# Kernel tuning notes

Measured on AMD Instinct MI355X. Metric: run time of the kernel, lower is better.

## Reference

```python
import jax, jax.numpy as jnp
import numpy as np

N, E = 50000, 800000
IN_DIM, DIM, MP_STEPS, POS_DIM = 64, 128, 3, 3
EPS = 1e-5


def _ln(v):
    # LayerNorm without affine params (elementwise_affine=False)
    m = jnp.mean(v, axis=-1, keepdims=True)
    var = jnp.mean((v - m) ** 2, axis=-1, keepdims=True)
    return (v - m) * jax.lax.rsqrt(var + EPS)


def setup_inputs() -> dict:
    key = jax.random.key(0)
    ks = jax.random.split(key, 10)
    x = jax.random.normal(ks[0], (N, IN_DIM), dtype=jnp.float32)
    pos = jax.random.normal(ks[1], (N, POS_DIM), dtype=jnp.float32)
    edge_index = jax.random.randint(ks[2], (2, E), 0, N, dtype=jnp.int64)
    # Linear embed: torch Linear stores [out,in]; we store transposed [in,out]
    s_e = 1.0 / np.sqrt(IN_DIM)
    embed_w = jax.random.uniform(ks[3], (IN_DIM, DIM), jnp.float32, -s_e, s_e)
    embed_b = jax.random.uniform(ks[4], (DIM,), jnp.float32, -s_e, s_e)
    s_m = 1.0 / np.sqrt(2 * DIM + POS_DIM)
    msg_w = jax.random.uniform(ks[5], (MP_STEPS, 2 * DIM + POS_DIM, DIM), jnp.float32, -s_m, s_m)
    msg_b = jax.random.uniform(ks[6], (MP_STEPS, DIM), jnp.float32, -s_m, s_m)
    s_u = 1.0 / np.sqrt(2 * DIM)
    upd_w = jax.random.uniform(ks[7], (MP_STEPS, 2 * DIM, DIM), jnp.float32, -s_u, s_u)
    upd_b = jax.random.uniform(ks[8], (MP_STEPS, DIM), jnp.float32, -s_u, s_u)
    return {"x": x, "pos": pos, "edge_index": edge_index,
            "embed_w": embed_w, "embed_b": embed_b,
            "msg_w": msg_w, "msg_b": msg_b,
            "upd_w": upd_w, "upd_b": upd_b}


def reference(x, pos, edge_index, embed_w, embed_b, msg_w, msg_b, upd_w, upd_b):
    row, col = edge_index[0], edge_index[1]
    h = x @ embed_w + embed_b  # [N, DIM]
    # edge_attr computed under torch.no_grad -> constant
    edge_attr = jax.lax.stop_gradient(pos[row] - pos[col])  # [E, POS_DIM]
    ones = jnp.ones((E,), dtype=h.dtype)
    counts = jax.ops.segment_sum(ones, col, num_segments=N)  # [N]
    denom = jnp.maximum(counts, 1.0)[:, None]
    for s in range(MP_STEPS):
        mi = jnp.concatenate([h[row], h[col], edge_attr], axis=-1)  # [E, 2D+3]
        messages = _ln(jax.nn.gelu(mi @ msg_w[s] + msg_b[s], approximate=False))
        agg = jax.ops.segment_sum(messages, col, num_segments=N) / denom  # scatter_mean
        ui = jnp.concatenate([h, agg], axis=-1)  # [N, 2D]
        h = h + _ln(ui @ upd_w[s] + upd_b[s])
    return h
```

## Files before the change

### kernel.cpp

```cpp
#include <hip/hip_runtime.h>
#include <hip/hip_bf16.h>

#define NN 50000
#define NE 800000
#define IND 64
#define DIM 128
#define KUPD 256
#define NB_SCAN 196
#define NTILE 3125

typedef __attribute__((ext_vector_type(8))) short bf16x8;
typedef __attribute__((ext_vector_type(4))) short bf16x4;
typedef __attribute__((ext_vector_type(4))) float f32x4;
typedef __attribute__((ext_vector_type(2))) float f32x2;

static __device__ __forceinline__ short f2bf(float f) {
  union { __hip_bfloat16 b; short s; } u;
  u.b = __float2bfloat16(f);
  return u.s;
}
static __device__ __forceinline__ float bf2f(unsigned short u) {
  union { float f; unsigned int i; } x; x.i = ((unsigned int)u) << 16; return x.f;
}
static __device__ __forceinline__ float fexp2(float x) {
  float r; asm("v_exp_f32 %0, %1" : "=v"(r) : "v"(x)); return r;
}
static __device__ __forceinline__ float frcp(float x) {
  float r; asm("v_rcp_f32 %0, %1" : "=v"(r) : "v"(x)); return r;
}
static __device__ __forceinline__ float qsum16(float x) {
  x += __int_as_float(__builtin_amdgcn_mov_dpp(__float_as_int(x), 0x128, 0xf, 0xf, false));
  x += __int_as_float(__builtin_amdgcn_mov_dpp(__float_as_int(x), 0x124, 0xf, 0xf, false));
  x += __int_as_float(__builtin_amdgcn_mov_dpp(__float_as_int(x), 0x122, 0xf, 0xf, false));
  x += __int_as_float(__builtin_amdgcn_mov_dpp(__float_as_int(x), 0x121, 0xf, 0xf, false));
  return x;
}

__global__ __launch_bounds__(256) void embed_kernel(
    const float* __restrict__ x, const float* __restrict__ w,
    const float* __restrict__ b, short* __restrict__ hb) {
  __shared__ float ws[IND * DIM];
  __shared__ float xs[8 * IND];
  const int t = threadIdx.x;
  for (int i = t * 4; i < IND * DIM; i += 1024)
    *(float4*)(ws + i) = *(const float4*)(w + i);
  {
    int i = t * 4;
    if (i < 8 * IND)
      *(float4*)(xs + i) = *(const float4*)(x + (size_t)blockIdx.x * (8 * IND) + i);
  }
  __syncthreads();
  const int d = t & 127, g = t >> 7;
  const float bd = b[d];
  for (int nnod = g; nnod < 8; nnod += 2) {
    float acc = bd;
#pragma unroll
    for (int k = 0; k < IND; ++k) acc += xs[nnod * IND + k] * ws[k * DIM + d];
    const size_t n = (size_t)blockIdx.x * 8 + nnod;
    hb[n * DIM + d] = f2bf(acc);
  }
}

__global__ __launch_bounds__(256) void counts_kernel(const int* __restrict__ ei,
                                                     int* __restrict__ cnt) {
  int e = blockIdx.x * 256 + threadIdx.x;
  if (e < NE) atomicAdd(&cnt[ei[NE + e]], 1);
}

__global__ __launch_bounds__(256) void bsum_dhist_kernel(const int* __restrict__ cnt,
                                                         int* __restrict__ bsum,
                                                         int* __restrict__ dhist) {
  __shared__ int lh[64];
  __shared__ int wsum[4];
  int t = threadIdx.x, idx = blockIdx.x * 256 + t;
  if (t < 64) lh[t] = 0;
  __syncthreads();
  int c = (idx < NN) ? cnt[idx] : 0;
  int s = c;
#pragma unroll
  for (int m = 1; m < 64; m <<= 1) s += __shfl_xor(s, m, 64);
  if ((t & 63) == 0) wsum[t >> 6] = s;
  if (idx < NN) {
    int d = c > 63 ? 63 : c;
    atomicAdd(&lh[63 - d], 1);
  }
  __syncthreads();
  if (t == 0) bsum[blockIdx.x] = wsum[0] + wsum[1] + wsum[2] + wsum[3];
  if (t < 64 && lh[t] > 0) atomicAdd(&dhist[t], lh[t]);
}

__global__ __launch_bounds__(256) void bscan_dscan_kernel(const int* __restrict__ bsum,
                                                          int* __restrict__ boff,
                                                          const int* __restrict__ dhist,
                                                          int* __restrict__ dcur) {
  __shared__ int sh[256];
  int t = threadIdx.x;
  int v = (t < NB_SCAN) ? bsum[t] : 0;
  sh[t] = v;
  __syncthreads();
  for (int d = 1; d < 256; d <<= 1) {
    int u = (t >= d) ? sh[t - d] : 0;
    __syncthreads();
    sh[t] += u;
    __syncthreads();
  }
  if (t < NB_SCAN) boff[t] = sh[t] - v;
  if (t < 64) {
    int dv = dhist[t];
    int ds = dv;
    for (int d = 1; d < 64; d <<= 1) {
      int u = __shfl_up(ds, d, 64);
      if (t >= d) ds += u;
    }
    dcur[t] = ds - dv;
  }
}

__global__ __launch_bounds__(256) void final_scan_kernel(
    const int* __restrict__ cnt, const int* __restrict__ boff,
    int* __restrict__ dcur, const float* __restrict__ pos,
    int* __restrict__ off, int* __restrict__ cursor, float* __restrict__ rden,
    int* __restrict__ nodeOrd, float4* __restrict__ pos4g) {
  __shared__ int sh[256];
  __shared__ int lh[64];
  __shared__ int lbase[64];
  int b = blockIdx.x, t = threadIdx.x;
  int idx = b * 256 + t;
  bool act = (idx < NN);
  int c = act ? cnt[idx] : 0;
  if (t < 64) lh[t] = 0;
  sh[t] = c;
  __syncthreads();
  for (int d = 1; d < 256; d <<= 1) {
    int u = (t >= d) ? sh[t - d] : 0;
    __syncthreads();
    sh[t] += u;
    __syncthreads();
  }
  int bin = 63 - (c > 63 ? 63 : c);
  int lrank = 0;
  if (act) {
    int e = boff[b] + sh[t] - c;
    off[idx] = e;
    cursor[idx] = e;
    rden[idx] = 1.0f / fmaxf((float)c, 1.0f);
    pos4g[idx] = make_float4(pos[3 * idx], pos[3 * idx + 1], pos[3 * idx + 2], 0.f);
    lrank = atomicAdd(&lh[bin], 1);
  }
  __syncthreads();
  if (t < 64) lbase[t] = (lh[t] > 0) ? atomicAdd(&dcur[t], lh[t]) : 0;
  __syncthreads();
  if (act) nodeOrd[lbase[bin] + lrank] = idx;
  if (b == 0 && t == 0) off[NN] = NE;
}

__global__ __launch_bounds__(256) void scatter_kernel(const int* __restrict__ ei,
                                                      int* __restrict__ cursor,
                                                      int* __restrict__ rowOf) {
  int e = blockIdx.x * 256 + threadIdx.x;
  if (e < NE) {
    int c = ei[NE + e];
    int p = atomicAdd(&cursor[c], 1);
    rowOf[p] = ei[e];
  }
}

__global__ __launch_bounds__(256) void wt_all_kernel(const float* __restrict__ wm,
                                                     const float* __restrict__ wu,
                                                     short* __restrict__ wt12,
                                                     short* __restrict__ wtu) {
  int i = blockIdx.x * 256 + threadIdx.x;
  if (i < 3 * 256 * DIM) {
    int k = i % DIM, o = (i / DIM) % 256, s = i / (DIM * 256);
    int krow = (o < DIM) ? k : (DIM + k);
    int d = o & (DIM - 1);
    wt12[i] = f2bf(wm[((size_t)s * 259 + krow) * DIM + d]);
  } else {
    int j = i - 3 * 256 * DIM;
    if (j < 3 * DIM * KUPD) {
      int k = j % KUPD, d = (j / KUPD) % DIM, s = j / (KUPD * DIM);
      wtu[j] = f2bf(wu[((size_t)s * KUPD + k) * DIM + d]);
    }
  }
}

__global__ __launch_bounds__(512) void p12_kernel(const short* __restrict__ hb,
                                                  const short* __restrict__ wt12_s,
                                                  short* __restrict__ P12b) {
  __shared__ short wlds[256 * 132];
  const int t = threadIdx.x;
  const int wid = t >> 6, lane = t & 63;
  const int m = lane & 15, kg = lane >> 4;
  for (int i = t * 8; i < 256 * DIM; i += 512 * 8) {
    int r = i >> 7, c = i & 127;
    *(bf16x8*)(&wlds[r * 132 + c]) = *(const bf16x8*)(wt12_s + i);
  }
  __syncthreads();
  const int wgid = blockIdx.x * 8 + wid;
#pragma unroll
  for (int rep = 0; rep < 2; ++rep) {
    int tid = wgid + rep * 2048;
    if (tid >= NTILE) break;
    int nbase = tid * 16;
    const short* hrow = hb + (size_t)(nbase + m) * DIM;
    bf16x8 bfrag[4];
#pragma unroll
    for (int cc = 0; cc < 4; ++cc)
      bfrag[cc] = *(const bf16x8*)(hrow + cc * 32 + kg * 8);
#pragma unroll
    for (int half = 0; half < 2; ++half) {
      f32x4 acc[8];
#pragma unroll
      for (int i = 0; i < 8; ++i) acc[i] = (f32x4)0.0f;
#pragma unroll
      for (int cc = 0; cc < 4; ++cc) {
#pragma unroll
        for (int tl = 0; tl < 8; ++tl) {
          bf16x8 afrag = *(const bf16x8*)(&wlds[(half * DIM + tl * 16 + m) * 132 + cc * 32 + kg * 8]);
          acc[tl] = __builtin_amdgcn_mfma_f32_16x16x32_bf16(afrag, bfrag[cc], acc[tl], 0, 0, 0);
        }
      }
#pragma unroll
      for (int tl = 0; tl < 8; ++tl) {
        bf16x4 p;
#pragma unroll
        for (int j = 0; j < 4; ++j) p[j] = f2bf(acc[tl][j]);
        *(bf16x4*)(P12b + (size_t)(nbase + m) * 256 + half * DIM + tl * 16 + kg * 4) = p;
      }
    }
  }
}

__global__ __launch_bounds__(256) void msg_agg_kernel(
    const short* __restrict__ P12b, const float4* __restrict__ pos4g,
    const int* __restrict__ rowOf, const int* __restrict__ off,
    const int* __restrict__ nodeOrd, const float* __restrict__ rden,
    const float* __restrict__ wmsg_s,
    const float* __restrict__ bias_s, short* __restrict__ aggb) {
  const int t = threadIdx.x;
  const int wid = t >> 6, lane = t & 63;
  const int n = nodeOrd[blockIdx.x * 4 + wid];
  const int q = lane >> 4;
  const int d0 = (lane & 15) * 8;
  f32x2 w30v[4], w31v[4], w32v[4], pbv[4];
  {
    const float* w30p = wmsg_s + 256 * DIM + d0;
    const float* w31p = wmsg_s + 257 * DIM + d0;
    const float* w32p = wmsg_s + 258 * DIM + d0;
    bf16x8 p2v = *(const bf16x8*)(P12b + (size_t)n * 256 + DIM + d0);
#pragma unroll
    for (int p = 0; p < 4; ++p) {
      w30v[p] = *(const f32x2*)(w30p + 2 * p);
      w31v[p] = *(const f32x2*)(w31p + 2 * p);
      w32v[p] = *(const f32x2*)(w32p + 2 * p);
      f32x2 bb = *(const f32x2*)(bias_s + d0 + 2 * p);
      pbv[p].x = bf2f((unsigned short)p2v[2 * p]) + bb.x;
      pbv[p].y = bf2f((unsigned short)p2v[2 * p + 1]) + bb.y;
    }
  }
  const float4 pc = pos4g[n];
  const int start = off[n], end = off[n + 1];
  f32x2 av[4];
#pragma unroll
  for (int p = 0; p < 4; ++p) av[p] = (f32x2)0.0f;
  float bacc = 0.f;
  const f32x2 gc1 = (f32x2)(-0.102951604f);
  const f32x2 gc0 = (f32x2)(-2.30234934f);
  const f32x2 onev = (f32x2)1.0f;
  if (start < end) {
    const int last = end - 1;
    int ia = start + q; if (ia > last) ia = last;
    int ra = rowOf[ia];
    bf16x8 p1a = *(const bf16x8*)(P12b + (size_t)ra * 256 + d0);
    float4 ppa = pos4g[ra];
    int ib = start + 4 + q; if (ib > last) ib = last;
    int rb = rowOf[ib];
    bf16x8 p1b = *(const bf16x8*)(P12b + (size_t)rb * 256 + d0);
    float4 ppb = pos4g[rb];
#pragma unroll 2
    for (int jg = start; jg < end; jg += 4) {
      int ic = jg + 8 + q; if (ic > last) ic = last;
      int rc = rowOf[ic];
      bf16x8 p1c = *(const bf16x8*)(P12b + (size_t)rc * 256 + d0);
      float4 ppc = pos4g[rc];
      f32x2 e0v = (f32x2)(ppa.x - pc.x);
      f32x2 e1v = (f32x2)(ppa.y - pc.y);
      f32x2 e2v = (f32x2)(ppa.z - pc.z);
      f32x2 g[4];
      f32x2 s1v = (f32x2)0.0f, s2v = (f32x2)0.0f;
#pragma unroll
      for (int p = 0; p < 4; ++p) {
        unsigned int u = ((const unsigned int*)&p1a)[p];
        f32x2 v;
        v.x = __uint_as_float(u << 16);
        v.y = __uint_as_float(u & 0xffff0000u);
        v = v + pbv[p];
        v = __builtin_elementwise_fma(e2v, w32v[p], v);
        v = __builtin_elementwise_fma(e1v, w31v[p], v);
        v = __builtin_elementwise_fma(e0v, w30v[p], v);
        f32x2 u2 = v * v;
        f32x2 wv = __builtin_elementwise_fma(u2, gc1, gc0);
        f32x2 zv = v * wv;
        f32x2 tv;
        tv.x = fexp2(zv.x);
        tv.y = fexp2(zv.y);
        tv = tv + onev;
        f32x2 rv;
        rv.x = frcp(tv.x);
        rv.y = frcp(tv.y);
        f32x2 gg = v * rv;
        g[p] = gg;
        s1v = s1v + gg;
        s2v = __builtin_elementwise_fma(gg, gg, s2v);
      }
      float s1 = s1v.x + s1v.y;
      float s2 = s2v.x + s2v.y;
      s1 = qsum16(s1);
      s2 = qsum16(s2);
      float mean = s1 * (1.0f / 128.0f);
      float tvv = fmaf(mean, -mean, 1e-5f);
      float var = fmaf(s2, 1.0f / 128.0f, tvv);
      float rstd = rsqrtf(var);
      float rs = (jg + q < end) ? rstd : 0.0f;
      bacc = fmaf(mean, rs, bacc);
      f32x2 rsv = (f32x2)rs;
#pragma unroll
      for (int p = 0; p < 4; ++p) av[p] = __builtin_elementwise_fma(g[p], rsv, av[p]);
      p1a = p1b; ppa = ppb;
      p1b = p1c; ppb = ppc;
    }
  }
  const float rd = rden[n];
  float out[8];
#pragma unroll
  for (int p = 0; p < 4; ++p) {
    out[2 * p] = av[p].x - bacc;
    out[2 * p + 1] = av[p].y - bacc;
  }
  bf16x8 ob;
#pragma unroll
  for (int k = 0; k < 8; ++k) {
    out[k] += __shfl_xor(out[k], 16, 64);
    out[k] += __shfl_xor(out[k], 32, 64);
    ob[k] = f2bf(out[k] * rd);
  }
  if (q == 0)
    *(bf16x8*)(aggb + (size_t)n * DIM + d0) = ob;
}

template <int FINAL>
__global__ __launch_bounds__(512) void updp12_kernel(
    const short* hb, const short* __restrict__ aggb,
    const short* __restrict__ wtu_s,
    const short* __restrict__ wt12_n,
    const float* __restrict__ bias, float* __restrict__ h, short* hbo,
    short* __restrict__ P12b) {
  __shared__ short wlds[33792];
  const int t = threadIdx.x;
  const int wid = t >> 6, lane = t & 63;
  const int m = lane & 15, kg = lane >> 4;
  for (int i = t * 8; i < DIM * 256; i += 512 * 8) {
    int r = i >> 8, c = i & 255;
    *(bf16x8*)(&wlds[r * 264 + c]) = *(const bf16x8*)(wtu_s + i);
  }
  __syncthreads();
  const int wgid = blockIdx.x * 8 + wid;
#pragma unroll
  for (int rep = 0; rep < 2; ++rep) {
    int tid = wgid + rep * 2048;
    if (tid >= NTILE) break;
    int nbase = tid * 16;
    const int nA = nbase + m;
    const short* hrow = hb + (size_t)nA * DIM;
    const short* arow = aggb + (size_t)nA * DIM;

    f32x4 acc[8];
#pragma unroll
    for (int i = 0; i < 8; ++i) acc[i] = (f32x4)0.0f;
#pragma unroll
    for (int cc = 0; cc < 8; ++cc) {
      bf16x8 a = (cc < 4) ? *(const bf16x8*)(hrow + cc * 32 + kg * 8)
                          : *(const bf16x8*)(arow + (cc - 4) * 32 + kg * 8);
#pragma unroll
      for (int tl = 0; tl < 8; ++tl) {
        bf16x8 bfr = *(const bf16x8*)(&wlds[(tl * 16 + m) * 264 + cc * 32 + kg * 8]);
        acc[tl] = __builtin_amdgcn_mfma_f32_16x16x32_bf16(a, bfr, acc[tl], 0, 0, 0);
      }
    }

    float s1[4] = {0.f, 0.f, 0.f, 0.f}, s2[4] = {0.f, 0.f, 0.f, 0.f};
#pragma unroll
    for (int tl = 0; tl < 8; ++tl) {
      float bd = bias[tl * 16 + m];
#pragma unroll
      for (int j = 0; j < 4; ++j) {
        float xv = acc[tl][j] + bd;
        acc[tl][j] = xv;
        s1[j] += xv;
        s2[j] = fmaf(xv, xv, s2[j]);
      }
    }
#pragma unroll
    for (int mask = 1; mask < 16; mask <<= 1) {
#pragma unroll
      for (int j = 0; j < 4; ++j) {
        s1[j] += __shfl_xor(s1[j], mask, 64);
        s2[j] += __shfl_xor(s2[j], mask, 64);
      }
    }
#pragma unroll
    for (int j = 0; j < 4; ++j) {
      float mean = s1[j] * (1.0f / 128.0f);
      float var = s2[j] * (1.0f / 128.0f) - mean * mean;
      float rstd = rsqrtf(var + 1e-5f);
      int nw = nbase + kg * 4 + j;
#pragma unroll
      for (int tl = 0; tl < 8; ++tl) {
        int d = tl * 16 + m;
        float res = bf2f((unsigned short)hb[(size_t)nw * DIM + d]);
        float hv = res + (acc[tl][j] - mean) * rstd;
        if (FINAL) h[(size_t)nw * DIM + d] = hv;
        else       hbo[(size_t)nw * DIM + d] = f2bf(hv);
      }
    }
  }
  if (FINAL) return;

  __syncthreads();
  for (int i = t * 8; i < 256 * DIM; i += 512 * 8) {
    int r = i >> 7, c = i & 127;
    *(bf16x8*)(&wlds[r * 132 + c]) = *(const bf16x8*)(wt12_n + i);
  }
  __syncthreads();
#pragma unroll
  for (int rep = 0; rep < 2; ++rep) {
    int tid = wgid + rep * 2048;
    if (tid >= NTILE) break;
    int nbase = tid * 16;
    const short* hrow = hbo + (size_t)(nbase + m) * DIM;
    bf16x8 bfrag[4];
#pragma unroll
    for (int cc = 0; cc < 4; ++cc)
      bfrag[cc] = *(const bf16x8*)(hrow + cc * 32 + kg * 8);
#pragma unroll
    for (int half = 0; half < 2; ++half) {
      f32x4 acc[8];
#pragma unroll
      for (int i = 0; i < 8; ++i) acc[i] = (f32x4)0.0f;
#pragma unroll
      for (int cc = 0; cc < 4; ++cc) {
#pragma unroll
        for (int tl = 0; tl < 8; ++tl) {
          bf16x8 afrag = *(const bf16x8*)(&wlds[(half * DIM + tl * 16 + m) * 132 + cc * 32 + kg * 8]);
          acc[tl] = __builtin_amdgcn_mfma_f32_16x16x32_bf16(afrag, bfrag[cc], acc[tl], 0, 0, 0);
        }
      }
#pragma unroll
      for (int tl = 0; tl < 8; ++tl) {
        bf16x4 p;
#pragma unroll
        for (int j = 0; j < 4; ++j) p[j] = f2bf(acc[tl][j]);
        *(bf16x4*)(P12b + (size_t)(nbase + m) * 256 + half * DIM + tl * 16 + kg * 4) = p;
      }
    }
  }
}

extern "C" void kernel_launch(void* const* d_in, const int* in_sizes, int n_in,
                              void* d_out, int out_size, void* d_ws, size_t ws_size,
                              hipStream_t stream) {
  const float* x       = (const float*)d_in[0];
  const float* pos     = (const float*)d_in[1];
  const int* ei        = (const int*)d_in[2];
  const float* embed_w = (const float*)d_in[3];
  const float* embed_b = (const float*)d_in[4];
  const float* msg_w   = (const float*)d_in[5];
  const float* msg_b   = (const float*)d_in[6];
  const float* upd_w   = (const float*)d_in[7];
  const float* upd_b   = (const float*)d_in[8];
  float* h = (float*)d_out;

  char* ws = (char*)d_ws;
  size_t off_b = 0;
  short* hb     = (short*)(ws + off_b);  off_b += (size_t)NN * DIM * 2;
  short* P12b   = (short*)(ws + off_b);  off_b += (size_t)NN * 256 * 2;
  short* aggb   = (short*)(ws + off_b);  off_b += (size_t)NN * DIM * 2;
  float* rden   = (float*)(ws + off_b);  off_b += (size_t)NN * 4;
  int*   cnt    = (int*)(ws + off_b);    off_b += (size_t)NN * 4;
  int*   offs   = (int*)(ws + off_b);    off_b += (size_t)(NN + 16) * 4;
  int*   cursor = (int*)(ws + off_b);    off_b += (size_t)NN * 4;
  int*   rowOf  = (int*)(ws + off_b);    off_b += (size_t)(NE + 16) * 4;
  int*   bsum   = (int*)(ws + off_b);    off_b += (size_t)256 * 4;
  int*   boff   = (int*)(ws + off_b);    off_b += (size_t)256 * 4;
  int*   dhist  = (int*)(ws + off_b);    off_b += (size_t)64 * 4;
  int*   dcur   = (int*)(ws + off_b);    off_b += (size_t)64 * 4;
  int*   nodeOrd= (int*)(ws + off_b);    off_b += (size_t)NN * 4;
  float4* pos4g = (float4*)(ws + off_b); off_b += (size_t)NN * 16;
  short* wt12   = (short*)(ws + off_b);  off_b += (size_t)3 * 256 * DIM * 2;
  short* wtu    = (short*)(ws + off_b);  off_b += (size_t)3 * DIM * KUPD * 2;

  hipMemsetAsync(cnt, 0, (size_t)NN * 4, stream);
  hipMemsetAsync(dhist, 0, 64 * 4, stream);
  counts_kernel<<<(NE + 255) / 256, 256, 0, stream>>>(ei, cnt);
  bsum_dhist_kernel<<<NB_SCAN, 256, 0, stream>>>(cnt, bsum, dhist);
  bscan_dscan_kernel<<<1, 256, 0, stream>>>(bsum, boff, dhist, dcur);
  final_scan_kernel<<<NB_SCAN, 256, 0, stream>>>(cnt, boff, dcur, pos,
                                                 offs, cursor, rden, nodeOrd, pos4g);
  scatter_kernel<<<(NE + 255) / 256, 256, 0, stream>>>(ei, cursor, rowOf);
  wt_all_kernel<<<(3 * 256 * DIM + 3 * DIM * KUPD + 255) / 256, 256, 0, stream>>>(
      msg_w, upd_w, wt12, wtu);
  embed_kernel<<<NN / 8, 256, 0, stream>>>(x, embed_w, embed_b, hb);
  p12_kernel<<<256, 512, 0, stream>>>(hb, wt12, P12b);

  for (int s = 0; s < 3; ++s) {
    msg_agg_kernel<<<NN / 4, 256, 0, stream>>>(P12b, pos4g, rowOf, offs, nodeOrd, rden,
                                               msg_w + (size_t)s * 259 * DIM,
                                               msg_b + (size_t)s * DIM, aggb);
    if (s < 2)
      updp12_kernel<0><<<256, 512, 0, stream>>>(
          hb, aggb, wtu + (size_t)s * DIM * KUPD,
          wt12 + (size_t)(s + 1) * 256 * DIM,
          upd_b + (size_t)s * DIM, h, hb, P12b);
    else
      updp12_kernel<1><<<256, 512, 0, stream>>>(
          hb, aggb, wtu + (size_t)s * DIM * KUPD,
          wt12,
          upd_b + (size_t)s * DIM, h, hb, P12b);
  }
}
```

Measured before the change: 413.0 us.

## Fold edge position term into per-node projection to drop per-edge pos gathers

Splits the linear term pos[row]-pos[col] into a per-source part, computed inside the node-level P1 MFMA GEMM by appending pos as an extra K chunk, and a per-target part folded into the per-node bias in the message kernel. The edge loop then no longer gathers pos for each source or does three FMAs per feature. This removes a 16-byte random gather per edge and some VALU work, at the cost of a larger K in the P1 GEMM, more LDS use, and bf16 rounding of pos inside the projection, which slightly changes precision.

```diff
diff --git a/kernel.cpp b/kernel.cpp
--- a/kernel.cpp
+++ b/kernel.cpp
@@ -8,6 +8,7 @@
 #define KUPD 256
 #define NB_SCAN 196
 #define NTILE 3125
+#define W12S 36864
 
 typedef __attribute__((ext_vector_type(8))) short bf16x8;
 typedef __attribute__((ext_vector_type(4))) short bf16x4;
@@ -170,13 +171,22 @@
                                                      short* __restrict__ wt12,
                                                      short* __restrict__ wtu) {
   int i = blockIdx.x * 256 + threadIdx.x;
-  if (i < 3 * 256 * DIM) {
-    int k = i % DIM, o = (i / DIM) % 256, s = i / (DIM * 256);
-    int krow = (o < DIM) ? k : (DIM + k);
-    int d = o & (DIM - 1);
-    wt12[i] = f2bf(wm[((size_t)s * 259 + krow) * DIM + d]);
+  if (i < 3 * W12S) {
+    int s = i / W12S, r = i % W12S;
+    float val;
+    if (r < 128 * 160) {
+      int o = r / 160, k = r % 160;
+      if (k < 128)      val = wm[((size_t)s * 259 + k) * DIM + o];
+      else if (k < 131) val = wm[((size_t)s * 259 + 256 + (k - 128)) * DIM + o];
+      else              val = 0.0f;
+    } else {
+      int r2 = r - 128 * 160;
+      int o = r2 >> 7, k = r2 & 127;
+      val = wm[((size_t)s * 259 + 128 + k) * DIM + o];
+    }
+    wt12[i] = f2bf(val);
   } else {
-    int j = i - 3 * 256 * DIM;
+    int j = i - 3 * W12S;
     if (j < 3 * DIM * KUPD) {
       int k = j % KUPD, d = (j / KUPD) % DIM, s = j / (KUPD * DIM);
       wtu[j] = f2bf(wu[((size_t)s * KUPD + k) * DIM + d]);
@@ -186,14 +196,21 @@
 
 __global__ __launch_bounds__(512) void p12_kernel(const short* __restrict__ hb,
                                                   const short* __restrict__ wt12_s,
+                                                  const float4* __restrict__ pos4g,
                                                   short* __restrict__ P12b) {
-  __shared__ short wlds[256 * 132];
+  __shared__ short wlds[128 * 164 + 128 * 132];
+  short* l0 = wlds;
+  short* l1 = wlds + 128 * 164;
   const int t = threadIdx.x;
   const int wid = t >> 6, lane = t & 63;
   const int m = lane & 15, kg = lane >> 4;
-  for (int i = t * 8; i < 256 * DIM; i += 512 * 8) {
+  for (int i = t * 8; i < 128 * 160; i += 512 * 8) {
+    int r = i / 160, c = i % 160;
+    *(bf16x8*)(&l0[r * 164 + c]) = *(const bf16x8*)(wt12_s + i);
+  }
+  for (int i = t * 8; i < 128 * 128; i += 512 * 8) {
     int r = i >> 7, c = i & 127;
-    *(bf16x8*)(&wlds[r * 132 + c]) = *(const bf16x8*)(wt12_s + i);
+    *(bf16x8*)(&l1[r * 132 + c]) = *(const bf16x8*)(wt12_s + 128 * 160 + i);
   }
   __syncthreads();
   const int wgid = blockIdx.x * 8 + wid;
@@ -203,20 +220,27 @@
     if (tid >= NTILE) break;
     int nbase = tid * 16;
     const short* hrow = hb + (size_t)(nbase + m) * DIM;
-    bf16x8 bfrag[4];
+    bf16x8 bfrag[5];
 #pragma unroll
     for (int cc = 0; cc < 4; ++cc)
       bfrag[cc] = *(const bf16x8*)(hrow + cc * 32 + kg * 8);
-#pragma unroll
-    for (int half = 0; half < 2; ++half) {
+    {
+      bf16x8 b4 = (bf16x8)0;
+      if (kg == 0) {
+        float4 pp = pos4g[nbase + m];
+        b4[0] = f2bf(pp.x); b4[1] = f2bf(pp.y); b4[2] = f2bf(pp.z);
+      }
+      bfrag[4] = b4;
+    }
+    {
       f32x4 acc[8];
 #pragma unroll
       for (int i = 0; i < 8; ++i) acc[i] = (f32x4)0.0f;
 #pragma unroll
-      for (int cc = 0; cc < 4; ++cc) {
+      for (int cc = 0; cc < 5; ++cc) {
 #pragma unroll
         for (int tl = 0; tl < 8; ++tl) {
-          bf16x8 afrag = *(const bf16x8*)(&wlds[(half * DIM + tl * 16 + m) * 132 + cc * 32 + kg * 8]);
+          bf16x8 afrag = *(const bf16x8*)(&l0[(tl * 16 + m) * 164 + cc * 32 + kg * 8]);
           acc[tl] = __builtin_amdgcn_mfma_f32_16x16x32_bf16(afrag, bfrag[cc], acc[tl], 0, 0, 0);
         }
       }
@@ -225,14 +249,35 @@
         bf16x4 p;
 #pragma unroll
         for (int j = 0; j < 4; ++j) p[j] = f2bf(acc[tl][j]);
-        *(bf16x4*)(P12b + (size_t)(nbase + m) * 256 + half * DIM + tl * 16 + kg * 4) = p;
+        *(bf16x4*)(P12b + (size_t)(nbase + m) * 256 + tl * 16 + kg * 4) = p;
+      }
+    }
+    {
+      f32x4 acc[8];
+#pragma unroll
+      for (int i = 0; i < 8; ++i) acc[i] = (f32x4)0.0f;
+#pragma unroll
+      for (int cc = 0; cc < 4; ++cc) {
+#pragma unroll
+        for (int tl = 0; tl < 8; ++tl) {
+          bf16x8 afrag = *(const bf16x8*)(&l1[(tl * 16 + m) * 132 + cc * 32 + kg * 8]);
+          acc[tl] = __builtin_amdgcn_mfma_f32_16x16x32_bf16(afrag, bfrag[cc], acc[tl], 0, 0, 0);
+        }
+      }
+#pragma unroll
+      for (int tl = 0; tl < 8; ++tl) {
+        bf16x4 p;
+#pragma unroll
+        for (int j = 0; j < 4; ++j) p[j] = f2bf(acc[tl][j]);
+        *(bf16x4*)(P12b + (size_t)(nbase + m) * 256 + DIM + tl * 16 + kg * 4) = p;
       }
     }
   }
 }
 
 __global__ __launch_bounds__(256) void msg_agg_kernel(
-    const short* __restrict__ P12b, const float4* __restrict__ pos4g,
+    const short* __restrict__ P12b,
+    const float4* __restrict__ pos4g,
     const int* __restrict__ rowOf, const int* __restrict__ off,
     const int* __restrict__ nodeOrd, const float* __restrict__ rden,
     const float* __restrict__ wmsg_s,
@@ -242,23 +287,25 @@
   const int n = nodeOrd[blockIdx.x * 4 + wid];
   const int q = lane >> 4;
   const int d0 = (lane & 15) * 8;
-  f32x2 w30v[4], w31v[4], w32v[4], pbv[4];
+  f32x2 pbv[4];
   {
+    const float4 pc = pos4g[n];
     const float* w30p = wmsg_s + 256 * DIM + d0;
     const float* w31p = wmsg_s + 257 * DIM + d0;
     const float* w32p = wmsg_s + 258 * DIM + d0;
     bf16x8 p2v = *(const bf16x8*)(P12b + (size_t)n * 256 + DIM + d0);
 #pragma unroll
     for (int p = 0; p < 4; ++p) {
-      w30v[p] = *(const f32x2*)(w30p + 2 * p);
-      w31v[p] = *(const f32x2*)(w31p + 2 * p);
-      w32v[p] = *(const f32x2*)(w32p + 2 * p);
+      f32x2 w0 = *(const f32x2*)(w30p + 2 * p);
+      f32x2 w1 = *(const f32x2*)(w31p + 2 * p);
+      f32x2 w2 = *(const f32x2*)(w32p + 2 * p);
       f32x2 bb = *(const f32x2*)(bias_s + d0 + 2 * p);
-      pbv[p].x = bf2f((unsigned short)p2v[2 * p]) + bb.x;
-      pbv[p].y = bf2f((unsigned short)p2v[2 * p + 1]) + bb.y;
-    }
-  }
-  const float4 pc = pos4g[n];
+      pbv[p].x = bf2f((unsigned short)p2v[2 * p]) + bb.x
+                 - (pc.x * w0.x + pc.y * w1.x + pc.z * w2.x);
+      pbv[p].y = bf2f((unsigned short)p2v[2 * p + 1]) + bb.y
+                 - (pc.x * w0.y + pc.y * w1.y + pc.z * w2.y);
+    }
+  }
   const int start = off[n], end = off[n + 1];
   f32x2 av[4];
 #pragma unroll
@@ -272,20 +319,14 @@
     int ia = start + q; if (ia > last) ia = last;
     int ra = rowOf[ia];
     bf16x8 p1a = *(const bf16x8*)(P12b + (size_t)ra * 256 + d0);
-    float4 ppa = pos4g[ra];
     int ib = start + 4 + q; if (ib > last) ib = last;
     int rb = rowOf[ib];
     bf16x8 p1b = *(const bf16x8*)(P12b + (size_t)rb * 256 + d0);
-    float4 ppb = pos4g[rb];
 #pragma unroll 2
     for (int jg = start; jg < end; jg += 4) {
       int ic = jg + 8 + q; if (ic > last) ic = last;
       int rc = rowOf[ic];
       bf16x8 p1c = *(const bf16x8*)(P12b + (size_t)rc * 256 + d0);
-      float4 ppc = pos4g[rc];
-      f32x2 e0v = (f32x2)(ppa.x - pc.x);
-      f32x2 e1v = (f32x2)(ppa.y - pc.y);
-      f32x2 e2v = (f32x2)(ppa.z - pc.z);
       f32x2 g[4];
       f32x2 s1v = (f32x2)0.0f, s2v = (f32x2)0.0f;
 #pragma unroll
@@ -295,9 +336,6 @@
         v.x = __uint_as_float(u << 16);
         v.y = __uint_as_float(u & 0xffff0000u);
         v = v + pbv[p];
-        v = __builtin_elementwise_fma(e2v, w32v[p], v);
-        v = __builtin_elementwise_fma(e1v, w31v[p], v);
-        v = __builtin_elementwise_fma(e0v, w30v[p], v);
         f32x2 u2 = v * v;
         f32x2 wv = __builtin_elementwise_fma(u2, gc1, gc0);
         f32x2 zv = v * wv;
@@ -326,8 +364,8 @@
       f32x2 rsv = (f32x2)rs;
 #pragma unroll
       for (int p = 0; p < 4; ++p) av[p] = __builtin_elementwise_fma(g[p], rsv, av[p]);
-      p1a = p1b; ppa = ppb;
-      p1b = p1c; ppb = ppc;
+      p1a = p1b;
+      p1b = p1c;
     }
   }
   const float rd = rden[n];
@@ -353,9 +391,10 @@
     const short* hb, const short* __restrict__ aggb,
     const short* __restrict__ wtu_s,
     const short* __restrict__ wt12_n,
+    const float4* __restrict__ pos4g,
     const float* __restrict__ bias, float* __restrict__ h, short* hbo,
     short* __restrict__ P12b) {
-  __shared__ short wlds[33792];
+  __shared__ short wlds[128 * 164 + 128 * 132];
   const int t = threadIdx.x;
   const int wid = t >> 6, lane = t & 63;
   const int m = lane & 15, kg = lane >> 4;
@@ -427,9 +466,15 @@
   if (FINAL) return;
 
   __syncthreads();
-  for (int i = t * 8; i < 256 * DIM; i += 512 * 8) {
+  short* l0 = wlds;
+  short* l1 = wlds + 128 * 164;
+  for (int i = t * 8; i < 128 * 160; i += 512 * 8) {
+    int r = i / 160, c = i % 160;
+    *(bf16x8*)(&l0[r * 164 + c]) = *(const bf16x8*)(wt12_n + i);
+  }
+  for (int i = t * 8; i < 128 * 128; i += 512 * 8) {
     int r = i >> 7, c = i & 127;
-    *(bf16x8*)(&wlds[r * 132 + c]) = *(const bf16x8*)(wt12_n + i);
+    *(bf16x8*)(&l1[r * 132 + c]) = *(const bf16x8*)(wt12_n + 128 * 160 + i);
   }
   __syncthreads();
 #pragma unroll
@@ -438,20 +483,27 @@
     if (tid >= NTILE) break;
     int nbase = tid * 16;
     const short* hrow = hbo + (size_t)(nbase + m) * DIM;
-    bf16x8 bfrag[4];
+    bf16x8 bfrag[5];
 #pragma unroll
     for (int cc = 0; cc < 4; ++cc)
       bfrag[cc] = *(const bf16x8*)(hrow + cc * 32 + kg * 8);
-#pragma unroll
-    for (int half = 0; half < 2; ++half) {
+    {
+      bf16x8 b4 = (bf16x8)0;
+      if (kg == 0) {
+        float4 pp = pos4g[nbase + m];
+        b4[0] = f2bf(pp.x); b4[1] = f2bf(pp.y); b4[2] = f2bf(pp.z);
+      }
+      bfrag[4] = b4;
+    }
+    {
       f32x4 acc[8];
 #pragma unroll
       for (int i = 0; i < 8; ++i) acc[i] = (f32x4)0.0f;
 #pragma unroll
-      for (int cc = 0; cc < 4; ++cc) {
+      for (int cc = 0; cc < 5; ++cc) {
 #pragma unroll
         for (int tl = 0; tl < 8; ++tl) {
-          bf16x8 afrag = *(const bf16x8*)(&wlds[(half * DIM + tl * 16 + m) * 132 + cc * 32 + kg * 8]);
+          bf16x8 afrag = *(const bf16x8*)(&l0[(tl * 16 + m) * 164 + cc * 32 + kg * 8]);
           acc[tl] = __builtin_amdgcn_mfma_f32_16x16x32_bf16(afrag, bfrag[cc], acc[tl], 0, 0, 0);
         }
       }
@@ -460,7 +512,27 @@
         bf16x4 p;
 #pragma unroll
         for (int j = 0; j < 4; ++j) p[j] = f2bf(acc[tl][j]);
-        *(bf16x4*)(P12b + (size_t)(nbase + m) * 256 + half * DIM + tl * 16 + kg * 4) = p;
+        *(bf16x4*)(P12b + (size_t)(nbase + m) * 256 + tl * 16 + kg * 4) = p;
+      }
+    }
+    {
+      f32x4 acc[8];
+#pragma unroll
+      for (int i = 0; i < 8; ++i) acc[i] = (f32x4)0.0f;
+#pragma unroll
+      for (int cc = 0; cc < 4; ++cc) {
+#pragma unroll
+        for (int tl = 0; tl < 8; ++tl) {
+          bf16x8 afrag = *(const bf16x8*)(&l1[(tl * 16 + m) * 132 + cc * 32 + kg * 8]);
+          acc[tl] = __builtin_amdgcn_mfma_f32_16x16x32_bf16(afrag, bfrag[cc], acc[tl], 0, 0, 0);
+        }
+      }
+#pragma unroll
+      for (int tl = 0; tl < 8; ++tl) {
+        bf16x4 p;
+#pragma unroll
+        for (int j = 0; j < 4; ++j) p[j] = f2bf(acc[tl][j]);
+        *(bf16x4*)(P12b + (size_t)(nbase + m) * 256 + DIM + tl * 16 + kg * 4) = p;
       }
     }
   }
@@ -496,7 +568,7 @@
   int*   dcur   = (int*)(ws + off_b);    off_b += (size_t)64 * 4;
   int*   nodeOrd= (int*)(ws + off_b);    off_b += (size_t)NN * 4;
   float4* pos4g = (float4*)(ws + off_b); off_b += (size_t)NN * 16;
-  short* wt12   = (short*)(ws + off_b);  off_b += (size_t)3 * 256 * DIM * 2;
+  short* wt12   = (short*)(ws + off_b);  off_b += (size_t)3 * W12S * 2;
   short* wtu    = (short*)(ws + off_b);  off_b += (size_t)3 * DIM * KUPD * 2;
 
   hipMemsetAsync(cnt, 0, (size_t)NN * 4, stream);
@@ -507,10 +579,10 @@
   final_scan_kernel<<<NB_SCAN, 256, 0, stream>>>(cnt, boff, dcur, pos,
                                                  offs, cursor, rden, nodeOrd, pos4g);
   scatter_kernel<<<(NE + 255) / 256, 256, 0, stream>>>(ei, cursor, rowOf);
-  wt_all_kernel<<<(3 * 256 * DIM + 3 * DIM * KUPD + 255) / 256, 256, 0, stream>>>(
+  wt_all_kernel<<<(3 * W12S + 3 * DIM * KUPD + 255) / 256, 256, 0, stream>>>(
       msg_w, upd_w, wt12, wtu);
   embed_kernel<<<NN / 8, 256, 0, stream>>>(x, embed_w, embed_b, hb);
-  p12_kernel<<<256, 512, 0, stream>>>(hb, wt12, P12b);
+  p12_kernel<<<256, 512, 0, stream>>>(hb, wt12, pos4g, P12b);
 
   for (int s = 0; s < 3; ++s) {
     msg_agg_kernel<<<NN / 4, 256, 0, stream>>>(P12b, pos4g, rowOf, offs, nodeOrd, rden,
@@ -519,12 +591,12 @@
     if (s < 2)
       updp12_kernel<0><<<256, 512, 0, stream>>>(
           hb, aggb, wtu + (size_t)s * DIM * KUPD,
-          wt12 + (size_t)(s + 1) * 256 * DIM,
+          wt12 + (size_t)(s + 1) * W12S, pos4g,
           upd_b + (size_t)s * DIM, h, hb, P12b);
     else
       updp12_kernel<1><<<256, 512, 0, stream>>>(
           hb, aggb, wtu + (size_t)s * DIM * KUPD,
-          wt12,
+          wt12, pos4g,
           upd_b + (size_t)s * DIM, h, hb, P12b);
   }
 }
```

Measured after the change: 461.5 us. +11.7%, slower.

## Fold edge position term into per-node projections, drop per-edge pos gathers

Applied to the files above, without the earlier changes.

Because edge_attr = pos[row] - pos[col] enters linearly, the pos·W3 term is split into a per-source-node part, added to P1 in the projection kernels, and a per-destination part, subtracted once from the node bias in msg_agg. This removes the per-edge float4 pos gather and three FMAs per element from the hot edge loop. In exchange the position contribution is now rounded to bf16 together with P1, which slightly changes numerics, and the projection kernels do a little extra work and LDS staging.

```diff
diff --git a/kernel.cpp b/kernel.cpp
--- a/kernel.cpp
+++ b/kernel.cpp
@@ -186,8 +186,11 @@
 
 __global__ __launch_bounds__(512) void p12_kernel(const short* __restrict__ hb,
                                                   const short* __restrict__ wt12_s,
+                                                  const float4* __restrict__ pos4g,
+                                                  const float* __restrict__ w3,
                                                   short* __restrict__ P12b) {
   __shared__ short wlds[256 * 132];
+  __shared__ float w3lds[384];
   const int t = threadIdx.x;
   const int wid = t >> 6, lane = t & 63;
   const int m = lane & 15, kg = lane >> 4;
@@ -195,6 +198,7 @@
     int r = i >> 7, c = i & 127;
     *(bf16x8*)(&wlds[r * 132 + c]) = *(const bf16x8*)(wt12_s + i);
   }
+  if (t < 384) w3lds[t] = w3[t];
   __syncthreads();
   const int wgid = blockIdx.x * 8 + wid;
 #pragma unroll
@@ -203,6 +207,7 @@
     if (tid >= NTILE) break;
     int nbase = tid * 16;
     const short* hrow = hb + (size_t)(nbase + m) * DIM;
+    const float4 pp = pos4g[nbase + m];
     bf16x8 bfrag[4];
 #pragma unroll
     for (int cc = 0; cc < 4; ++cc)
@@ -224,7 +229,14 @@
       for (int tl = 0; tl < 8; ++tl) {
         bf16x4 p;
 #pragma unroll
-        for (int j = 0; j < 4; ++j) p[j] = f2bf(acc[tl][j]);
+        for (int j = 0; j < 4; ++j) {
+          float val = acc[tl][j];
+          if (half == 0) {
+            int o = tl * 16 + kg * 4 + j;
+            val += pp.x * w3lds[o] + pp.y * w3lds[128 + o] + pp.z * w3lds[256 + o];
+          }
+          p[j] = f2bf(val);
+        }
         *(bf16x4*)(P12b + (size_t)(nbase + m) * 256 + half * DIM + tl * 16 + kg * 4) = p;
       }
     }
@@ -232,7 +244,8 @@
 }
 
 __global__ __launch_bounds__(256) void msg_agg_kernel(
-    const short* __restrict__ P12b, const float4* __restrict__ pos4g,
+    const short* __restrict__ P12b,
+    const float4* __restrict__ pos4g,
     const int* __restrict__ rowOf, const int* __restrict__ off,
     const int* __restrict__ nodeOrd, const float* __restrict__ rden,
     const float* __restrict__ wmsg_s,
@@ -242,23 +255,25 @@
   const int n = nodeOrd[blockIdx.x * 4 + wid];
   const int q = lane >> 4;
   const int d0 = (lane & 15) * 8;
-  f32x2 w30v[4], w31v[4], w32v[4], pbv[4];
+  f32x2 pbv[4];
   {
+    const float4 pc = pos4g[n];
     const float* w30p = wmsg_s + 256 * DIM + d0;
     const float* w31p = wmsg_s + 257 * DIM + d0;
     const float* w32p = wmsg_s + 258 * DIM + d0;
     bf16x8 p2v = *(const bf16x8*)(P12b + (size_t)n * 256 + DIM + d0);
 #pragma unroll
     for (int p = 0; p < 4; ++p) {
-      w30v[p] = *(const f32x2*)(w30p + 2 * p);
-      w31v[p] = *(const f32x2*)(w31p + 2 * p);
-      w32v[p] = *(const f32x2*)(w32p + 2 * p);
+      f32x2 w0 = *(const f32x2*)(w30p + 2 * p);
+      f32x2 w1 = *(const f32x2*)(w31p + 2 * p);
+      f32x2 w2 = *(const f32x2*)(w32p + 2 * p);
       f32x2 bb = *(const f32x2*)(bias_s + d0 + 2 * p);
-      pbv[p].x = bf2f((unsigned short)p2v[2 * p]) + bb.x;
-      pbv[p].y = bf2f((unsigned short)p2v[2 * p + 1]) + bb.y;
-    }
-  }
-  const float4 pc = pos4g[n];
+      pbv[p].x = bf2f((unsigned short)p2v[2 * p]) + bb.x
+                 - (pc.x * w0.x + pc.y * w1.x + pc.z * w2.x);
+      pbv[p].y = bf2f((unsigned short)p2v[2 * p + 1]) + bb.y
+                 - (pc.x * w0.y + pc.y * w1.y + pc.z * w2.y);
+    }
+  }
   const int start = off[n], end = off[n + 1];
   f32x2 av[4];
 #pragma unroll
@@ -272,20 +287,14 @@
     int ia = start + q; if (ia > last) ia = last;
     int ra = rowOf[ia];
     bf16x8 p1a = *(const bf16x8*)(P12b + (size_t)ra * 256 + d0);
-    float4 ppa = pos4g[ra];
     int ib = start + 4 + q; if (ib > last) ib = last;
     int rb = rowOf[ib];
     bf16x8 p1b = *(const bf16x8*)(P12b + (size_t)rb * 256 + d0);
-    float4 ppb = pos4g[rb];
 #pragma unroll 2
     for (int jg = start; jg < end; jg += 4) {
       int ic = jg + 8 + q; if (ic > last) ic = last;
       int rc = rowOf[ic];
       bf16x8 p1c = *(const bf16x8*)(P12b + (size_t)rc * 256 + d0);
-      float4 ppc = pos4g[rc];
-      f32x2 e0v = (f32x2)(ppa.x - pc.x);
-      f32x2 e1v = (f32x2)(ppa.y - pc.y);
-      f32x2 e2v = (f32x2)(ppa.z - pc.z);
       f32x2 g[4];
       f32x2 s1v = (f32x2)0.0f, s2v = (f32x2)0.0f;
 #pragma unroll
@@ -295,9 +304,6 @@
         v.x = __uint_as_float(u << 16);
         v.y = __uint_as_float(u & 0xffff0000u);
         v = v + pbv[p];
-        v = __builtin_elementwise_fma(e2v, w32v[p], v);
-        v = __builtin_elementwise_fma(e1v, w31v[p], v);
-        v = __builtin_elementwise_fma(e0v, w30v[p], v);
         f32x2 u2 = v * v;
         f32x2 wv = __builtin_elementwise_fma(u2, gc1, gc0);
         f32x2 zv = v * wv;
@@ -326,8 +332,8 @@
       f32x2 rsv = (f32x2)rs;
 #pragma unroll
       for (int p = 0; p < 4; ++p) av[p] = __builtin_elementwise_fma(g[p], rsv, av[p]);
-      p1a = p1b; ppa = ppb;
-      p1b = p1c; ppb = ppc;
+      p1a = p1b;
+      p1b = p1c;
     }
   }
   const float rd = rden[n];
@@ -353,9 +359,12 @@
     const short* hb, const short* __restrict__ aggb,
     const short* __restrict__ wtu_s,
     const short* __restrict__ wt12_n,
+    const float4* __restrict__ pos4g,
+    const float* __restrict__ w3_n,
     const float* __restrict__ bias, float* __restrict__ h, short* hbo,
     short* __restrict__ P12b) {
   __shared__ short wlds[33792];
+  __shared__ float w3lds[384];
   const int t = threadIdx.x;
   const int wid = t >> 6, lane = t & 63;
   const int m = lane & 15, kg = lane >> 4;
@@ -363,6 +372,7 @@
     int r = i >> 8, c = i & 255;
     *(bf16x8*)(&wlds[r * 264 + c]) = *(const bf16x8*)(wtu_s + i);
   }
+  if (!FINAL && t < 384) w3lds[t] = w3_n[t];
   __syncthreads();
   const int wgid = blockIdx.x * 8 + wid;
 #pragma unroll
@@ -438,6 +448,7 @@
     if (tid >= NTILE) break;
     int nbase = tid * 16;
     const short* hrow = hbo + (size_t)(nbase + m) * DIM;
+    const float4 pp = pos4g[nbase + m];
     bf16x8 bfrag[4];
 #pragma unroll
     for (int cc = 0; cc < 4; ++cc)
@@ -459,7 +470,14 @@
       for (int tl = 0; tl < 8; ++tl) {
         bf16x4 p;
 #pragma unroll
-        for (int j = 0; j < 4; ++j) p[j] = f2bf(acc[tl][j]);
+        for (int j = 0; j < 4; ++j) {
+          float val = acc[tl][j];
+          if (half == 0) {
+            int o = tl * 16 + kg * 4 + j;
+            val += pp.x * w3lds[o] + pp.y * w3lds[128 + o] + pp.z * w3lds[256 + o];
+          }
+          p[j] = f2bf(val);
+        }
         *(bf16x4*)(P12b + (size_t)(nbase + m) * 256 + half * DIM + tl * 16 + kg * 4) = p;
       }
     }
@@ -510,7 +528,7 @@
   wt_all_kernel<<<(3 * 256 * DIM + 3 * DIM * KUPD + 255) / 256, 256, 0, stream>>>(
       msg_w, upd_w, wt12, wtu);
   embed_kernel<<<NN / 8, 256, 0, stream>>>(x, embed_w, embed_b, hb);
-  p12_kernel<<<256, 512, 0, stream>>>(hb, wt12, P12b);
+  p12_kernel<<<256, 512, 0, stream>>>(hb, wt12, pos4g, msg_w + 256 * DIM, P12b);
 
   for (int s = 0; s < 3; ++s) {
     msg_agg_kernel<<<NN / 4, 256, 0, stream>>>(P12b, pos4g, rowOf, offs, nodeOrd, rden,
@@ -519,12 +537,13 @@
     if (s < 2)
       updp12_kernel<0><<<256, 512, 0, stream>>>(
           hb, aggb, wtu + (size_t)s * DIM * KUPD,
-          wt12 + (size_t)(s + 1) * 256 * DIM,
+          wt12 + (size_t)(s + 1) * 256 * DIM, pos4g,
+          msg_w + (size_t)(s + 1) * 259 * DIM + 256 * DIM,
           upd_b + (size_t)s * DIM, h, hb, P12b);
     else
       updp12_kernel<1><<<256, 512, 0, stream>>>(
           hb, aggb, wtu + (size_t)s * DIM * KUPD,
-          wt12,
+          wt12, pos4g, msg_w,
           upd_b + (size_t)s * DIM, h, hb, P12b);
   }
 }
```

Result: faster. 393.8 us (-4.7%).
